# Kernel tuning notes

Measured on AMD Instinct MI355X. Metric: run time of the kernel, lower is better.

Reference implementation:

```python
import jax, jax.numpy as jnp
import numpy as np
from jax import lax

NL = 4        # n_layers
V = 32000     # vocab_size
D = 768       # embedding_dim (d_model)
L = 2048      # seq_len
B = 1         # batch
E = 1536      # d_inner = expand * d_model
N = 8         # d_state
R = 48        # dt_rank = ceil(768/16)
K = 3         # d_conv


def rmsnorm(x, w, eps=1e-6):
    return x * w * lax.rsqrt(jnp.mean(x * x, axis=-1, keepdims=True) + eps)


def causal_dwconv(x, w, b):
    # depthwise causal conv1d; x: (B,L,E), w: (K,E), b: (E,)
    xp = jnp.pad(x, ((0, 0), (K - 1, 0), (0, 0)))
    y = sum(xp[:, k:k + x.shape[1], :] * w[k] for k in range(K))
    return y + b


def selective_scan(dt, A, Bm, C, u):
    # dt,u: (B,L,E); A: (E,N); Bm,C: (B,L,N)
    dA = jnp.exp(dt[..., None] * A)                      # (B,L,E,N)
    dBu = dt[..., None] * Bm[:, :, None, :] * u[..., None]  # (B,L,E,N)

    def step(h, xs):
        a, bu, c = xs
        h = a * h + bu                                   # (B,E,N)
        return h, jnp.einsum('ben,bn->be', h, c)

    h0 = jnp.zeros((u.shape[0], E, N), u.dtype)
    _, ys = lax.scan(step, h0, (dA.swapaxes(0, 1), dBu.swapaxes(0, 1), C.swapaxes(0, 1)))
    return ys.swapaxes(0, 1)                             # (B,L,E)


def mamba_block(x, Wi, bi, cw, cb, Wx, Wdt, bdt, Alog, Dsk, Wo, bo):
    xz = x @ Wi + bi                                     # (B,L,2E)
    u, res = jnp.split(xz, 2, axis=-1)
    u = jax.nn.silu(causal_dwconv(u, cw, cb))
    dbl = u @ Wx                                         # (B,L,R+2N)
    dt, Bm, C = dbl[..., :R], dbl[..., R:R + N], dbl[..., R + N:]
    dt = jax.nn.softplus(dt @ Wdt + bdt)                 # (B,L,E)
    A = -jnp.exp(Alog)                                   # (E,N)
    y = selective_scan(dt, A, Bm, C, u) + u * Dsk
    y = y * jax.nn.silu(res)
    return y @ Wo + bo


def setup_inputs() -> dict:
    key = jax.random.key(0)
    ks = jax.random.split(key, 10)
    s = 0.02
    return {
        'inputs': jax.random.randint(ks[0], (B, L), 0, V),
        'emb': jax.random.normal(ks[1], (V, D), jnp.float32) * s,
        'W_in': jax.random.normal(ks[2], (NL, D, 2 * E), jnp.float32) * s,
        'b_in': jnp.zeros((NL, 2 * E), jnp.float32),
        'conv_w': jax.random.normal(ks[3], (NL, K, E), jnp.float32) * s,
        'conv_b': jnp.zeros((NL, E), jnp.float32),
        'W_x': jax.random.normal(ks[4], (NL, E, R + 2 * N), jnp.float32) * s,
        'W_dt': jax.random.normal(ks[5], (NL, R, E), jnp.float32) * s,
        'b_dt': jax.random.normal(ks[6], (NL, E), jnp.float32) * s,
        'A_log': jnp.tile(jnp.log(jnp.arange(1, N + 1, dtype=jnp.float32)), (NL, E, 1)),
        'D_skip': jnp.ones((NL, E), jnp.float32),
        'W_out': jax.random.normal(ks[7], (NL, E, D), jnp.float32) * s,
        'b_out': jnp.zeros((NL, D), jnp.float32),
        'norm_w': jnp.ones((NL, D), jnp.float32),
        'normf_w': jnp.ones((D,), jnp.float32),
        'W_lm': jax.random.normal(ks[8], (D, V), jnp.float32) * s,
    }


def reference(inputs, emb, W_in, b_in, conv_w, conv_b, W_x, W_dt, b_dt, A_log, D_skip, W_out, b_out, norm_w, normf_w, W_lm):
    x = emb[inputs]                                      # (B,L,D)
    for i in range(NL):
        x = x + mamba_block(rmsnorm(x, norm_w[i]), W_in[i], b_in[i], conv_w[i], conv_b[i],
                            W_x[i], W_dt[i], b_dt[i], A_log[i], D_skip[i], W_out[i], b_out[i])
    x = rmsnorm(x, normf_w)
    return x @ W_lm                                      # logits (B,L,V)
```

## Files before the change

### kernel.cpp

```cpp
#include <hip/hip_runtime.h>
#include <hip/hip_bf16.h>
#include <cstdint>
#include <cstddef>

#define L_SEQ 2048
#define DIM   768
#define EDIM  1536
#define NLAY  4
#define NST   8
#define RNK   48
#define VOC   32000
#define NCH   64
#define CHS   32
#define TT    16

typedef __bf16 bf16x8 __attribute__((ext_vector_type(8)));
typedef float  f32x4  __attribute__((ext_vector_type(4)));

typedef __attribute__((address_space(3))) void lds_void;
typedef const __attribute__((address_space(1))) void gbl_void;

__device__ __forceinline__ void gld_lds16(const void* g, void* l) {
    __builtin_amdgcn_global_load_lds((gbl_void*)g, (lds_void*)l, 16, 0, 0);
}

__device__ __forceinline__ float bf2f(__hip_bfloat16 v) { return __bfloat162float(v); }

__global__ __launch_bounds__(256)
void tcvt_k(const float* __restrict__ src, __hip_bfloat16* __restrict__ dst,
            int R, int C, size_t sstride, size_t dstride)
{
    src += (size_t)blockIdx.z * sstride;
    dst += (size_t)blockIdx.z * dstride;
    __shared__ float tile[32][33];
    const int c0 = blockIdx.x * 32, r0 = blockIdx.y * 32;
    const int tx = threadIdx.x & 31;
    const int ty = threadIdx.x >> 5;
#pragma unroll
    for (int j = 0; j < 32; j += 8)
        tile[ty + j][tx] = src[(size_t)(r0 + ty + j) * C + c0 + tx];
    __syncthreads();
#pragma unroll
    for (int j = 0; j < 32; j += 8)
        dst[(size_t)(c0 + ty + j) * R + r0 + tx] = __float2bfloat16(tile[tx][ty + j]);
}

template<bool EMB>
__global__ __launch_bounds__(256)
void rmsnorm4_k(const float* __restrict__ src, const float* __restrict__ w,
                __hip_bfloat16* __restrict__ out,
                const int* __restrict__ ids, const float* __restrict__ emb,
                float* __restrict__ xcopy)
{
    const int row  = blockIdx.x * 4 + (threadIdx.x >> 6);
    const int lane = threadIdx.x & 63;
    const float* xr;
    if constexpr (EMB) xr = emb + (size_t)ids[row] * DIM;
    else               xr = src + (size_t)row * DIM;
    float v[12];
    float s = 0.f;
#pragma unroll
    for (int j = 0; j < 12; ++j) { v[j] = xr[lane + j * 64]; s += v[j] * v[j]; }
#pragma unroll
    for (int m = 32; m >= 1; m >>= 1) s += __shfl_xor(s, m, 64);
    const float sc = rsqrtf(s * (1.0f / DIM) + 1e-6f);
    __hip_bfloat16* o = out + (size_t)row * DIM;
#pragma unroll
    for (int j = 0; j < 12; ++j)
        o[lane + j * 64] = __float2bfloat16(v[j] * w[lane + j * 64] * sc);
    if constexpr (EMB) {
        float* xc = xcopy + (size_t)row * DIM;
#pragma unroll
        for (int j = 0; j < 12; ++j) xc[lane + j * 64] = v[j];
    }
}

template<int EPI, int BM, int BN, int BK, typename OT>
__global__ __launch_bounds__(256)
void gemm_bf16(const __hip_bfloat16* __restrict__ A,
               const __hip_bfloat16* __restrict__ BT,
               const float* __restrict__ bias,
               OT* __restrict__ C,
               int M, int N, int K)
{
    constexpr int WM = BM / 2, WN = BN / 2;
    constexpr int MF = WM / 16, NF = WN / 16;
    constexpr int AOPS = BM * BK * 2 / 4096;
    constexpr int BOPS = BN * BK * 2 / 4096;
    static_assert(AOPS + BOPS == 4, "vmcnt literal assumes 4 ops/stage");

    __shared__ __hip_bfloat16 As[2][BM * BK];
    __shared__ __hip_bfloat16 Bs[2][BN * BK];

    const int tid  = threadIdx.x;
    const int lane = tid & 63, wid = tid >> 6;
    const int wr = wid >> 1, wc = wid & 1;

    const int nwg = gridDim.x;
    int wg = blockIdx.x;
    if ((nwg & 7) == 0) wg = (wg & 7) * (nwg >> 3) + (wg >> 3);
    const int mblks = M / BM;
    const int m0 = (wg % mblks) * BM;
    const int n0 = (wg / mblks) * BN;

    f32x4 acc[MF][NF] = {};

    auto stage = [&](int b, int k0) {
#pragma unroll
        for (int i = 0; i < AOPS; ++i) {
            int row, colE;
            if constexpr (BK == 32) { row = i * 64 + (tid >> 2); colE = (((tid & 3) ^ ((tid >> 3) & 3)) << 3); }
            else                    { row = i * 32 + (tid >> 3); colE = (((tid & 7) ^ ((tid >> 3) & 7)) << 3); }
            gld_lds16(A + (size_t)(m0 + row) * K + k0 + colE,
                      (char*)As[b] + i * 4096 + wid * 1024);
        }
#pragma unroll
        for (int i = 0; i < BOPS; ++i) {
            int row, colE;
            if constexpr (BK == 32) { row = i * 64 + (tid >> 2); colE = (((tid & 3) ^ ((tid >> 3) & 3)) << 3); }
            else                    { row = i * 32 + (tid >> 3); colE = (((tid & 7) ^ ((tid >> 3) & 7)) << 3); }
            gld_lds16(BT + (size_t)(n0 + row) * K + k0 + colE,
                      (char*)Bs[b] + i * 4096 + wid * 1024);
        }
    };

    const int NT = K / BK;
    stage(0, 0);

    const int rr   = lane & 15;
    const int kq16 = (lane >> 4) << 4;

    for (int kt = 0; kt < NT; ++kt) {
        const int cur = kt & 1;
        if (kt + 1 < NT) {
            stage(cur ^ 1, (kt + 1) * BK);
            asm volatile("s_waitcnt vmcnt(4)" ::: "memory");
        } else {
            asm volatile("s_waitcnt vmcnt(0)" ::: "memory");
        }
        __syncthreads();

        const char* AsB = (const char*)As[cur];
        const char* BsB = (const char*)Bs[cur];
#pragma unroll
        for (int ks = 0; ks < BK / 32; ++ks) {
            bf16x8 af[MF], bfr[NF];
#pragma unroll
            for (int m = 0; m < MF; ++m) {
                const int row = wr * WM + m * 16 + rr;
                const int swz = (BK == 32) ? (((row >> 1) & 3) << 4) : ((row & 7) << 4);
                af[m] = *(const bf16x8*)(AsB + ((row * (BK * 2) + ks * 64 + kq16) ^ swz));
            }
#pragma unroll
            for (int n = 0; n < NF; ++n) {
                const int row = wc * WN + n * 16 + rr;
                const int swz = (BK == 32) ? (((row >> 1) & 3) << 4) : ((row & 7) << 4);
                bfr[n] = *(const bf16x8*)(BsB + ((row * (BK * 2) + ks * 64 + kq16) ^ swz));
            }
#pragma unroll
            for (int m = 0; m < MF; ++m)
#pragma unroll
                for (int n = 0; n < NF; ++n)
                    acc[m][n] = __builtin_amdgcn_mfma_f32_16x16x32_bf16(af[m], bfr[n], acc[m][n], 0, 0, 0);
        }
        __syncthreads();
    }

    const int row0 = m0 + wr * WM + ((lane >> 4) * 4);
    const int col0 = n0 + wc * WN + (lane & 15);
#pragma unroll
    for (int m = 0; m < MF; ++m)
#pragma unroll
        for (int n = 0; n < NF; ++n) {
            const int c = col0 + n * 16;
#pragma unroll
            for (int j = 0; j < 4; ++j) {
                const int r = row0 + m * 16 + j;
                const float v = acc[m][n][j];
                const size_t o = (size_t)r * N + c;
                if constexpr (EPI == 0) {
                    const float z = v + bias[c];
                    if constexpr (__is_same(OT, float)) C[o] = z;
                    else                                C[o] = __float2bfloat16(z);
                } else {
                    C[o] += v + bias[c];
                }
            }
        }
}

__global__ __launch_bounds__(512, 2)
void gemm8_bf16(const __hip_bfloat16* __restrict__ A,
                const __hip_bfloat16* __restrict__ BT,
                float* __restrict__ C,
                int M, int N, int K)
{
    __shared__ uint4 lds_u4[8192];
    char* Aring = (char*)lds_u4;
    char* Bring = (char*)lds_u4 + 65536;

    const int tid  = threadIdx.x;
    const int lane = tid & 63, wid = tid >> 6;
    const int wr = wid >> 2, wc = wid & 3;

    const int nwg = gridDim.x;
    int wg = blockIdx.x;
    if ((nwg & 7) == 0) wg = (wg & 7) * (nwg >> 3) + (wg >> 3);
    const int mblks = M >> 8;
    const int m0 = (wg % mblks) * 256;
    const int n0 = (wg / mblks) * 256;
    const int NT = K >> 6;

    const int rA   = wid * 8 + (lane >> 3);
    const int colE = (((lane & 7) ^ ((lane >> 3) & 7)) << 3);
    const int ldsb = wid * 1024;

    const int rr   = lane & 15;
    const int kq16 = (lane >> 4) << 4;
    const int rbB  = (wc & 1) * 64;

    f32x4 acc[8][4] = {};
    bf16x8 areg[4][2], breg[4][2];

#define STAGE8(SRC, BASE0, TL, TC, H, RING)                                           \
    {                                                                                 \
        const int _slot = ((2 * (TL) + (H)) & 3);                                     \
        const __hip_bfloat16* _g = (SRC) + (size_t)((BASE0) + (H) * 128 + rA) * K     \
                                        + (size_t)(TC) * 64 + colE;                   \
        char* _l = (RING) + _slot * 16384 + ldsb;                                     \
        gld_lds16(_g, _l);                                                            \
        gld_lds16(_g + (size_t)64 * K, _l + 8192);                                    \
    }

#define READ_A8(MH)                                                                   \
    _Pragma("unroll")                                                                 \
    for (int _m = 0; _m < 4; ++_m) {                                                  \
        _Pragma("unroll")                                                             \
        for (int _ks = 0; _ks < 2; ++_ks) {                                           \
            const int _rh = (MH) * 64 + _m * 16 + rr;                                 \
            const int _by = (_rh * 128 + _ks * 64 + kq16) ^ ((_rh & 7) << 4);         \
            areg[_m][_ks] = *(const bf16x8*)(sAp + _by);                              \
        }                                                                             \
    }

#define READ_B8(NH)                                                                   \
    _Pragma("unroll")                                                                 \
    for (int _n = 0; _n < 2; ++_n) {                                                  \
        _Pragma("unroll")                                                             \
        for (int _ks = 0; _ks < 2; ++_ks) {                                           \
            const int _rh = rbB + (NH) * 32 + _n * 16 + rr;                           \
            const int _by = (_rh * 128 + _ks * 64 + kq16) ^ ((_rh & 7) << 4);         \
            breg[(NH) * 2 + _n][_ks] = *(const bf16x8*)(sBp + _by);                   \
        }                                                                             \
    }

#define MFMA_QUAD8(MH, NH)                                                            \
    __builtin_amdgcn_s_setprio(1);                                                    \
    _Pragma("unroll")                                                                 \
    for (int _ks = 0; _ks < 2; ++_ks)                                                 \
        _Pragma("unroll")                                                             \
        for (int _m = 0; _m < 4; ++_m)                                                \
            _Pragma("unroll")                                                         \
            for (int _n = 0; _n < 2; ++_n)                                            \
                acc[(MH) * 4 + _m][(NH) * 2 + _n] =                                   \
                    __builtin_amdgcn_mfma_f32_16x16x32_bf16(                          \
                        areg[_m][_ks], breg[(NH) * 2 + _n][_ks],                      \
                        acc[(MH) * 4 + _m][(NH) * 2 + _n], 0, 0, 0);                  \
    __builtin_amdgcn_s_setprio(0);

    STAGE8(A,  m0, 0, 0, 0, Aring);
    STAGE8(A,  m0, 0, 0, 1, Aring);
    STAGE8(BT, n0, 0, 0, 0, Bring);
    STAGE8(BT, n0, 0, 0, 1, Bring);
    {
        const int t1p = (NT > 1) ? 1 : 0;
        STAGE8(BT, n0, 1, t1p, 0, Bring);
        STAGE8(BT, n0, 1, t1p, 1, Bring);
    }
    asm volatile("s_waitcnt vmcnt(4)" ::: "memory");
    __builtin_amdgcn_s_barrier();

    for (int kt = 0; kt < NT; ++kt) {
        const char* sAp = Aring + (((2 * kt + wr) & 3) << 14);
        const char* sBp = Bring + (((2 * kt + (wc >> 1)) & 3) << 14);
        const int tn1 = (kt + 1 < NT) ? kt + 1 : NT - 1;
        const int tn2 = (kt + 2 < NT) ? kt + 2 : NT - 1;

        READ_A8(0)
        READ_B8(0)
        STAGE8(A, m0, kt + 1, tn1, 0, Aring);
        __builtin_amdgcn_s_barrier();
        MFMA_QUAD8(0, 0)
        __builtin_amdgcn_s_barrier();

        READ_B8(1)
        STAGE8(A, m0, kt + 1, tn1, 1, Aring);
        __builtin_amdgcn_s_barrier();
        MFMA_QUAD8(0, 1)
        __builtin_amdgcn_s_barrier();

        READ_A8(1)
        STAGE8(BT, n0, kt + 2, tn2, 0, Bring);
        __builtin_amdgcn_s_barrier();
        MFMA_QUAD8(1, 0)
        __builtin_amdgcn_s_barrier();

        STAGE8(BT, n0, kt + 2, tn2, 1, Bring);
        __builtin_amdgcn_s_barrier();
        MFMA_QUAD8(1, 1)
        asm volatile("s_waitcnt vmcnt(4)" ::: "memory");
        __builtin_amdgcn_s_barrier();
    }

    const int row0 = m0 + wr * 128 + ((lane >> 4) * 4);
    const int col0 = n0 + wc * 64 + (lane & 15);
#pragma unroll
    for (int m = 0; m < 8; ++m)
#pragma unroll
        for (int n = 0; n < 4; ++n) {
            const int c = col0 + n * 16;
#pragma unroll
            for (int j = 0; j < 4; ++j)
                C[(size_t)(row0 + m * 16 + j) * N + c] = acc[m][n][j];
        }
#undef STAGE8
#undef READ_A8
#undef READ_B8
#undef MFMA_QUAD8
}

__global__ __launch_bounds__(256)
void mid_k(const __hip_bfloat16* __restrict__ xz, const float* __restrict__ cw,
           const float* __restrict__ cb, const __hip_bfloat16* __restrict__ WxT,
           const float* __restrict__ Wdt, const float* __restrict__ bdt,
           __hip_bfloat16* __restrict__ u_f, float* __restrict__ dbl,
           float* __restrict__ dtb)
{
    __shared__ __hip_bfloat16 us[TT][EDIM + 8];
    __shared__ float dbs[TT][64];
    const int tid = threadIdx.x;
    const int t0  = blockIdx.x * TT;

#pragma unroll
    for (int j = 0; j < EDIM / 256; ++j) {
        const int e = tid + j * 256;
        const float w0 = cw[e], w1 = cw[EDIM + e], w2 = cw[2 * EDIM + e], b = cb[e];
        float xm2 = (t0 >= 2) ? bf2f(xz[(size_t)(t0 - 2) * (2 * EDIM) + e]) : 0.f;
        float xm1 = (t0 >= 1) ? bf2f(xz[(size_t)(t0 - 1) * (2 * EDIM) + e]) : 0.f;
#pragma unroll
        for (int tt = 0; tt < TT; ++tt) {
            const float xc = bf2f(xz[(size_t)(t0 + tt) * (2 * EDIM) + e]);
            float a = b + w0 * xm2 + w1 * xm1 + w2 * xc;
            a = a / (1.f + __expf(-a));
            const __hip_bfloat16 ab = __float2bfloat16(a);
            us[tt][e] = ab;
            u_f[(size_t)(t0 + tt) * EDIM + e] = ab;
            xm2 = xm1; xm1 = xc;
        }
    }
    __syncthreads();

    {
        const int w = tid >> 6, lane = tid & 63;
        const int rr = lane & 15, kq = (lane >> 4) * 8;
        f32x4 acc = {};
        const __hip_bfloat16* bw = WxT + (size_t)(w * 16 + rr) * EDIM;
#pragma unroll 4
        for (int k0 = 0; k0 < EDIM; k0 += 32) {
            const bf16x8 af  = *(const bf16x8*)(&us[rr][k0 + kq]);
            const bf16x8 bfr = *(const bf16x8*)(bw + k0 + kq);
            acc = __builtin_amdgcn_mfma_f32_16x16x32_bf16(af, bfr, acc, 0, 0, 0);
        }
        const int nn = w * 16 + (lane & 15);
#pragma unroll
        for (int j = 0; j < 4; ++j) {
            const int tt2 = (lane >> 4) * 4 + j;
            dbs[tt2][nn] = acc[j];
            dbl[(size_t)(t0 + tt2) * 64 + nn] = acc[j];
        }
    }
    __syncthreads();

#pragma unroll 1
    for (int j = 0; j < EDIM / 256; ++j) {
        const int e = tid + j * 256;
        float wreg[RNK];
#pragma unroll
        for (int r = 0; r < RNK; ++r) wreg[r] = Wdt[(size_t)r * EDIM + e];
        const float b = bdt[e];
#pragma unroll 1
        for (int tt = 0; tt < TT; ++tt) {
            float acc = b;
#pragma unroll
            for (int r = 0; r < RNK; ++r) acc += dbs[tt][r] * wreg[r];
            const float ax = fabsf(acc);
            dtb[(size_t)(t0 + tt) * EDIM + e] = fmaxf(acc, 0.f) + log1pf(__expf(-ax));
        }
    }
}

__global__ __launch_bounds__(64)
void scanA_k(const float* __restrict__ dt, const __hip_bfloat16* __restrict__ u_f,
             const float* __restrict__ dbl, const float* __restrict__ alog,
             float* __restrict__ Pb, float* __restrict__ Hb)
{
    const int lane = threadIdx.x;
    const int e  = blockIdx.x * 64 + lane;
    const int c  = blockIdx.y;
    const int t0 = c * CHS;
    __shared__ float BC[CHS][16];
    if (lane < CHS) {
        const float4* s4 = (const float4*)(dbl + (size_t)(t0 + lane) * 64 + 48);
        float4* d4 = (float4*)(&BC[lane][0]);
        d4[0] = s4[0]; d4[1] = s4[1]; d4[2] = s4[2]; d4[3] = s4[3];
    }
    __syncthreads();
    float A8[NST], h[NST], P[NST];
#pragma unroll
    for (int n = 0; n < NST; ++n) {
        A8[n] = -__expf(alog[(size_t)e * NST + n]);
        h[n] = 0.f; P[n] = 1.f;
    }
    float pdt[8], pu[8];
#pragma unroll
    for (int j = 0; j < 8; ++j) {
        pdt[j] = dt [(size_t)(t0 + j) * EDIM + e];
        pu [j] = bf2f(u_f[(size_t)(t0 + j) * EDIM + e]);
    }
    for (int tb = 0; tb < CHS; tb += 8) {
        float cdt[8], cu[8];
#pragma unroll
        for (int j = 0; j < 8; ++j) { cdt[j] = pdt[j]; cu[j] = pu[j]; }
        if (tb + 8 < CHS) {
#pragma unroll
            for (int j = 0; j < 8; ++j) {
                pdt[j] = dt [(size_t)(t0 + tb + 8 + j) * EDIM + e];
                pu [j] = bf2f(u_f[(size_t)(t0 + tb + 8 + j) * EDIM + e]);
            }
        }
#pragma unroll
        for (int j = 0; j < 8; ++j) {
            const float du = cdt[j] * cu[j];
#pragma unroll
            for (int n = 0; n < NST; ++n) {
                const float dA = __expf(cdt[j] * A8[n]);
                h[n] = dA * h[n] + du * BC[tb + j][n];
                P[n] *= dA;
            }
        }
    }
    const size_t o = ((size_t)c * EDIM + e) * NST;
#pragma unroll
    for (int n = 0; n < NST; ++n) { Pb[o + n] = P[n]; Hb[o + n] = h[n]; }
}

__global__ __launch_bounds__(256)
void scanB_k(const float* __restrict__ Pb, const float* __restrict__ Hb,
             float* __restrict__ Hin)
{
    const int idx = blockIdx.x * 256 + threadIdx.x;
    float h = 0.f;
#pragma unroll 8
    for (int c = 0; c < NCH; ++c) {
        const size_t o = (size_t)c * EDIM * NST + idx;
        Hin[o] = h;
        h = Pb[o] * h + Hb[o];
    }
}

__global__ __launch_bounds__(64)
void scanC_k(const float* __restrict__ dt, const __hip_bfloat16* __restrict__ u_f,
             const float* __restrict__ dbl, const float* __restrict__ alog,
             const float* __restrict__ Hin, const float* __restrict__ Dsk,
             const __hip_bfloat16* __restrict__ xz, __hip_bfloat16* __restrict__ ybf)
{
    const int lane = threadIdx.x;
    const int e  = blockIdx.x * 64 + lane;
    const int c  = blockIdx.y;
    const int t0 = c * CHS;
    __shared__ float BC[CHS][16];
    if (lane < CHS) {
        const float4* s4 = (const float4*)(dbl + (size_t)(t0 + lane) * 64 + 48);
        float4* d4 = (float4*)(&BC[lane][0]);
        d4[0] = s4[0]; d4[1] = s4[1]; d4[2] = s4[2]; d4[3] = s4[3];
    }
    __syncthreads();
    float A8[NST], h[NST];
#pragma unroll
    for (int n = 0; n < NST; ++n) {
        A8[n] = -__expf(alog[(size_t)e * NST + n]);
        h[n]  = Hin[(size_t)c * EDIM * NST + (size_t)e * NST + n];
    }
    const float Dv = Dsk[e];
    float pdt[8], pu[8], pr[8];
#pragma unroll
    for (int j = 0; j < 8; ++j) {
        pdt[j] = dt [(size_t)(t0 + j) * EDIM + e];
        pu [j] = bf2f(u_f[(size_t)(t0 + j) * EDIM + e]);
        pr [j] = bf2f(xz [(size_t)(t0 + j) * (2 * EDIM) + EDIM + e]);
    }
    for (int tb = 0; tb < CHS; tb += 8) {
        float cdt[8], cu[8], cr[8];
#pragma unroll
        for (int j = 0; j < 8; ++j) { cdt[j] = pdt[j]; cu[j] = pu[j]; cr[j] = pr[j]; }
        if (tb + 8 < CHS) {
#pragma unroll
            for (int j = 0; j < 8; ++j) {
                pdt[j] = dt [(size_t)(t0 + tb + 8 + j) * EDIM + e];
                pu [j] = bf2f(u_f[(size_t)(t0 + tb + 8 + j) * EDIM + e]);
                pr [j] = bf2f(xz [(size_t)(t0 + tb + 8 + j) * (2 * EDIM) + EDIM + e]);
            }
        }
#pragma unroll
        for (int j = 0; j < 8; ++j) {
            const float du = cdt[j] * cu[j];
            float y = 0.f;
#pragma unroll
            for (int n = 0; n < NST; ++n) {
                const float dA = __expf(cdt[j] * A8[n]);
                h[n] = dA * h[n] + du * BC[tb + j][n];
                y += h[n] * BC[tb + j][8 + n];
            }
            y += cu[j] * Dv;
            y *= cr[j] / (1.f + __expf(-cr[j]));
            ybf[(size_t)(t0 + tb + j) * EDIM + e] = __float2bfloat16(y);
        }
    }
}

extern "C" void kernel_launch(void* const* d_in, const int* in_sizes, int n_in,
                              void* d_out, int out_size, void* d_ws, size_t ws_size,
                              hipStream_t stream)
{
    const int*   ids     = (const int*)  d_in[0];
    const float* emb     = (const float*)d_in[1];
    const float* W_in    = (const float*)d_in[2];
    const float* b_in    = (const float*)d_in[3];
    const float* conv_w  = (const float*)d_in[4];
    const float* conv_b  = (const float*)d_in[5];
    const float* W_x     = (const float*)d_in[6];
    const float* W_dt    = (const float*)d_in[7];
    const float* b_dt    = (const float*)d_in[8];
    const float* A_log   = (const float*)d_in[9];
    const float* D_skip  = (const float*)d_in[10];
    const float* W_out   = (const float*)d_in[11];
    const float* b_out   = (const float*)d_in[12];
    const float* norm_w  = (const float*)d_in[13];
    const float* normf_w = (const float*)d_in[14];
    const float* W_lm    = (const float*)d_in[15];
    float* out = (float*)d_out;
    (void)in_sizes; (void)n_in; (void)out_size; (void)ws_size;

    char* ws = (char*)d_ws;
    size_t off = 0;
    auto alloc = [&](size_t b) -> void* {
        void* p = ws + off;
        off += (b + 255) & ~(size_t)255;
        return p;
    };
    __hip_bfloat16* WiT  = (__hip_bfloat16*)alloc((size_t)NLAY * 3072 * 768 * 2);
    __hip_bfloat16* WoT  = (__hip_bfloat16*)alloc((size_t)NLAY * 768 * 1536 * 2);
    __hip_bfloat16* WlmT = (__hip_bfloat16*)alloc((size_t)VOC * 768 * 2);
    __hip_bfloat16* WxT  = (__hip_bfloat16*)alloc((size_t)NLAY * 64 * EDIM * 2);
    float* x    = (float*)alloc((size_t)L_SEQ * DIM * 4);
    __hip_bfloat16* xn  = (__hip_bfloat16*)alloc((size_t)L_SEQ * DIM * 2);
    __hip_bfloat16* xz  = (__hip_bfloat16*)alloc((size_t)L_SEQ * 2 * EDIM * 2);
    __hip_bfloat16* u_f = (__hip_bfloat16*)alloc((size_t)L_SEQ * EDIM * 2);
    float* dblb = (float*)alloc((size_t)L_SEQ * 64 * 4);
    float* dtb  = (float*)alloc((size_t)L_SEQ * EDIM * 4);
    __hip_bfloat16* ybf = (__hip_bfloat16*)alloc((size_t)L_SEQ * EDIM * 2);
    float* Pb   = (float*)alloc((size_t)NCH * EDIM * NST * 4);
    float* Hb   = (float*)alloc((size_t)NCH * EDIM * NST * 4);
    float* Hin  = (float*)alloc((size_t)NCH * EDIM * NST * 4);

    tcvt_k<<<dim3(96, 24, NLAY), 256, 0, stream>>>(
        W_in, WiT, 768, 3072, (size_t)768 * 3072, (size_t)3072 * 768);
    tcvt_k<<<dim3(24, 48, NLAY), 256, 0, stream>>>(
        W_out, WoT, 1536, 768, (size_t)1536 * 768, (size_t)768 * 1536);
    tcvt_k<<<dim3(1000, 24, 1), 256, 0, stream>>>(
        W_lm, WlmT, 768, VOC, 0, 0);
    tcvt_k<<<dim3(2, 48, NLAY), 256, 0, stream>>>(
        W_x, WxT, EDIM, 64, (size_t)EDIM * 64, (size_t)64 * EDIM);

    rmsnorm4_k<true><<<dim3(L_SEQ / 4), 256, 0, stream>>>(
        nullptr, norm_w, xn, ids, emb, x);

    for (int l = 0; l < NLAY; ++l) {
        if (l > 0)
            rmsnorm4_k<false><<<dim3(L_SEQ / 4), 256, 0, stream>>>(
                x, norm_w + l * DIM, xn, nullptr, nullptr, nullptr);
        gemm_bf16<0, 128, 128, 32, __hip_bfloat16>
            <<<dim3((L_SEQ / 128) * (3072 / 128)), 256, 0, stream>>>(
            xn, WiT + (size_t)l * 3072 * 768, b_in + l * 2 * EDIM, xz, L_SEQ, 2 * EDIM, DIM);
        mid_k<<<dim3(L_SEQ / TT), 256, 0, stream>>>(
            xz, conv_w + l * 3 * EDIM, conv_b + l * EDIM,
            WxT + (size_t)l * 64 * EDIM,
            W_dt + (size_t)l * RNK * EDIM, b_dt + l * EDIM,
            u_f, dblb, dtb);
        scanA_k<<<dim3(EDIM / 64, NCH), 64, 0, stream>>>(
            dtb, u_f, dblb, A_log + (size_t)l * EDIM * NST, Pb, Hb);
        scanB_k<<<dim3(EDIM * NST / 256), 256, 0, stream>>>(Pb, Hb, Hin);
        scanC_k<<<dim3(EDIM / 64, NCH), 64, 0, stream>>>(
            dtb, u_f, dblb, A_log + (size_t)l * EDIM * NST, Hin, D_skip + l * EDIM, xz, ybf);
        gemm_bf16<1, 64, 64, 64, float>
            <<<dim3((L_SEQ / 64) * (768 / 64)), 256, 0, stream>>>(
            ybf, WoT + (size_t)l * 768 * 1536, b_out + l * DIM, x, L_SEQ, DIM, EDIM);
    }

    rmsnorm4_k<false><<<dim3(L_SEQ / 4), 256, 0, stream>>>(
        x, normf_w, xn, nullptr, nullptr, nullptr);
    gemm8_bf16<<<dim3((VOC / 256) * (L_SEQ / 256)), 512, 0, stream>>>(
        xn, WlmT, out, L_SEQ, VOC, DIM);
}
```

Before: 775.1 us.

## Fold inter-chunk scan into scanC and merge weight conversion launches

Removes the scanB kernel: each scanC block now recomputes its incoming chunk state by sequentially combining the Pb/Hb summaries of all preceding chunks, dropping one launch per layer and the Hin buffer. It also merges the four weight transpose/convert launches into a single prep kernel that dispatches on block index. The cost is redundant work: later chunks replay up to 63 prior summaries, which roughly multiplies the Pb/Hb reads across the grid, though these are small and likely cached.

```diff
diff --git a/kernel.cpp b/kernel.cpp
--- a/kernel.cpp
+++ b/kernel.cpp
@@ -27,13 +27,34 @@
 __device__ __forceinline__ float bf2f(__hip_bfloat16 v) { return __bfloat162float(v); }
 
 __global__ __launch_bounds__(256)
-void tcvt_k(const float* __restrict__ src, __hip_bfloat16* __restrict__ dst,
-            int R, int C, size_t sstride, size_t dstride)
-{
-    src += (size_t)blockIdx.z * sstride;
-    dst += (size_t)blockIdx.z * dstride;
+void prep_k(const float* __restrict__ W_in, const float* __restrict__ W_out,
+            const float* __restrict__ W_lm, const float* __restrict__ W_x,
+            __hip_bfloat16* __restrict__ WiT, __hip_bfloat16* __restrict__ WoT,
+            __hip_bfloat16* __restrict__ WlmT, __hip_bfloat16* __restrict__ WxT)
+{
     __shared__ float tile[32][33];
-    const int c0 = blockIdx.x * 32, r0 = blockIdx.y * 32;
+    int bid = blockIdx.x;
+    const float* src; __hip_bfloat16* dst;
+    int R, C, c0, r0;
+    if (bid < 9216) {
+        const int lz = bid / 2304, rem = bid % 2304;
+        R = 768; C = 3072; c0 = (rem % 96) * 32; r0 = (rem / 96) * 32;
+        src = W_in + (size_t)lz * 768 * 3072; dst = WiT + (size_t)lz * 3072 * 768;
+    } else if (bid < 9216 + 4608) {
+        bid -= 9216;
+        const int lz = bid / 1152, rem = bid % 1152;
+        R = 1536; C = 768; c0 = (rem % 24) * 32; r0 = (rem / 24) * 32;
+        src = W_out + (size_t)lz * 1536 * 768; dst = WoT + (size_t)lz * 768 * 1536;
+    } else if (bid < 9216 + 4608 + 24000) {
+        bid -= 9216 + 4608;
+        R = 768; C = 32000; c0 = (bid % 1000) * 32; r0 = (bid / 1000) * 32;
+        src = W_lm; dst = WlmT;
+    } else {
+        bid -= 9216 + 4608 + 24000;
+        const int lz = bid / 96, rem = bid % 96;
+        R = 1536; C = 64; c0 = (rem % 2) * 32; r0 = (rem / 2) * 32;
+        src = W_x + (size_t)lz * 1536 * 64; dst = WxT + (size_t)lz * 64 * 1536;
+    }
     const int tx = threadIdx.x & 31;
     const int ty = threadIdx.x >> 5;
 #pragma unroll
@@ -454,24 +475,11 @@
     for (int n = 0; n < NST; ++n) { Pb[o + n] = P[n]; Hb[o + n] = h[n]; }
 }
 
-__global__ __launch_bounds__(256)
-void scanB_k(const float* __restrict__ Pb, const float* __restrict__ Hb,
-             float* __restrict__ Hin)
-{
-    const int idx = blockIdx.x * 256 + threadIdx.x;
-    float h = 0.f;
-#pragma unroll 8
-    for (int c = 0; c < NCH; ++c) {
-        const size_t o = (size_t)c * EDIM * NST + idx;
-        Hin[o] = h;
-        h = Pb[o] * h + Hb[o];
-    }
-}
-
 __global__ __launch_bounds__(64)
 void scanC_k(const float* __restrict__ dt, const __hip_bfloat16* __restrict__ u_f,
              const float* __restrict__ dbl, const float* __restrict__ alog,
-             const float* __restrict__ Hin, const float* __restrict__ Dsk,
+             const float* __restrict__ Pb, const float* __restrict__ Hb,
+             const float* __restrict__ Dsk,
              const __hip_bfloat16* __restrict__ xz, __hip_bfloat16* __restrict__ ybf)
 {
     const int lane = threadIdx.x;
@@ -489,7 +497,18 @@
 #pragma unroll
     for (int n = 0; n < NST; ++n) {
         A8[n] = -__expf(alog[(size_t)e * NST + n]);
-        h[n]  = Hin[(size_t)c * EDIM * NST + (size_t)e * NST + n];
+        h[n]  = 0.f;
+    }
+    for (int cc = 0; cc < c; ++cc) {
+        const size_t o = ((size_t)cc * EDIM + e) * NST;
+        const float4 p0 = *(const float4*)(Pb + o);
+        const float4 p1 = *(const float4*)(Pb + o + 4);
+        const float4 q0 = *(const float4*)(Hb + o);
+        const float4 q1 = *(const float4*)(Hb + o + 4);
+        h[0] = p0.x * h[0] + q0.x;  h[1] = p0.y * h[1] + q0.y;
+        h[2] = p0.z * h[2] + q0.z;  h[3] = p0.w * h[3] + q0.w;
+        h[4] = p1.x * h[4] + q1.x;  h[5] = p1.y * h[5] + q1.y;
+        h[6] = p1.z * h[6] + q1.z;  h[7] = p1.w * h[7] + q1.w;
     }
     const float Dv = Dsk[e];
     float pdt[8], pu[8], pr[8];
@@ -571,16 +590,9 @@
     __hip_bfloat16* ybf = (__hip_bfloat16*)alloc((size_t)L_SEQ * EDIM * 2);
     float* Pb   = (float*)alloc((size_t)NCH * EDIM * NST * 4);
     float* Hb   = (float*)alloc((size_t)NCH * EDIM * NST * 4);
-    float* Hin  = (float*)alloc((size_t)NCH * EDIM * NST * 4);
-
-    tcvt_k<<<dim3(96, 24, NLAY), 256, 0, stream>>>(
-        W_in, WiT, 768, 3072, (size_t)768 * 3072, (size_t)3072 * 768);
-    tcvt_k<<<dim3(24, 48, NLAY), 256, 0, stream>>>(
-        W_out, WoT, 1536, 768, (size_t)1536 * 768, (size_t)768 * 1536);
-    tcvt_k<<<dim3(1000, 24, 1), 256, 0, stream>>>(
-        W_lm, WlmT, 768, VOC, 0, 0);
-    tcvt_k<<<dim3(2, 48, NLAY), 256, 0, stream>>>(
-        W_x, WxT, EDIM, 64, (size_t)EDIM * 64, (size_t)64 * EDIM);
+
+    prep_k<<<dim3(9216 + 4608 + 24000 + 384), 256, 0, stream>>>(
+        W_in, W_out, W_lm, W_x, WiT, WoT, WlmT, WxT);
 
     rmsnorm4_k<true><<<dim3(L_SEQ / 4), 256, 0, stream>>>(
         nullptr, norm_w, xn, ids, emb, x);
@@ -599,9 +611,9 @@
             u_f, dblb, dtb);
         scanA_k<<<dim3(EDIM / 64, NCH), 64, 0, stream>>>(
             dtb, u_f, dblb, A_log + (size_t)l * EDIM * NST, Pb, Hb);
-        scanB_k<<<dim3(EDIM * NST / 256), 256, 0, stream>>>(Pb, Hb, Hin);
         scanC_k<<<dim3(EDIM / 64, NCH), 64, 0, stream>>>(
-            dtb, u_f, dblb, A_log + (size_t)l * EDIM * NST, Hin, D_skip + l * EDIM, xz, ybf);
+            dtb, u_f, dblb, A_log + (size_t)l * EDIM * NST, Pb, Hb,
+            D_skip + l * EDIM, xz, ybf);
         gemm_bf16<1, 64, 64, 64, float>
             <<<dim3((L_SEQ / 64) * (768 / 64)), 256, 0, stream>>>(
             ybf, WoT + (size_t)l * 768 * 1536, b_out + l * DIM, x, L_SEQ, DIM, EDIM);
```

Result: no change. 788.3 us (+1.7%).
